# Performance work log

Hardware: AMD Instinct MI355X
Metric: run time of the kernel (lower is better)

Reference implementation:

```python
import math
import jax, jax.numpy as jnp
import numpy as np

B, S, HID, H, NREL = 4, 512, 1024, 16, 64
D = HID // H  # per-head size = 64, must equal relation embedding dim


def setup_inputs() -> dict:
    key = jax.random.key(0)
    ks = jax.random.split(key, 12)
    w = lambda k, shape: jax.random.normal(k, shape, jnp.float32) * 0.02
    return {
        "q_in": jax.random.normal(ks[0], (B, S, HID), jnp.float32),
        "k_in": jax.random.normal(ks[1], (B, S, HID), jnp.float32),
        "v_in": jax.random.normal(ks[2], (B, S, HID), jnp.float32),
        "mask": jax.random.randint(ks[3], (B, 1, S, S), 0, NREL),
        "Wq": w(ks[4], (HID, HID)), "bq": jnp.zeros((HID,), jnp.float32),
        "Wk": w(ks[5], (HID, HID)), "bk": jnp.zeros((HID,), jnp.float32),
        "Wv": w(ks[6], (HID, HID)), "bv": jnp.zeros((HID,), jnp.float32),
        "Wo": w(ks[7], (HID, HID)), "bo": jnp.zeros((HID,), jnp.float32),
        "rel_k_table": w(ks[8], (NREL, D)),
        "rel_v_table": w(ks[9], (NREL, D)),
    }


def reference(q_in, k_in, v_in, mask, Wq, bq, Wk, bk, Wv, bv, Wo, bo,
              rel_k_table, rel_v_table):
    def proj(x, W, b):  # [B,S,HID] -> [B,H,S,D]
        return (x @ W.T + b).reshape(B, S, H, D).transpose(0, 2, 1, 3)

    q = proj(q_in, Wq, bq)
    k = proj(k_in, Wk, bk)
    v = proj(v_in, Wv, bv)

    ids = mask[:, 0]                      # [B,S,S] relation ids
    rel_k = rel_k_table[ids]              # [B,S,S,D]
    rel_v = rel_v_table[ids]              # [B,S,S,D]

    scores = jnp.einsum('bhqd,bhkd->bhqk', q, k)
    scores = scores + jnp.einsum('bhqd,bqkd->bhqk', q, rel_k) / 4.0
    scores = scores / math.sqrt(float(D))

    bias = (1.0 - (mask > 0).astype(scores.dtype)) * -10000.0  # [B,1,S,S]
    probs = jax.nn.softmax(scores + bias, axis=-1)             # [B,H,S,S]

    out = jnp.einsum('bhqk,bhkd->bhqd', probs, v)
    out = out + 0.25 * jnp.einsum('bhqk,bqkd->bhqd', probs, rel_v)
    out = out.transpose(0, 2, 1, 3).reshape(B, S, HID)
    return out @ Wo.T + bo
```

## Files before the change

kernel.cpp:

```cpp
#include <hip/hip_runtime.h>


typedef __attribute__((ext_vector_type(8))) short bf16x8 __attribute__((may_alias));
typedef __attribute__((ext_vector_type(4))) float f32x4;

__device__ __forceinline__ short f2bf(float x) {
    unsigned u = __float_as_uint(x);
    u += 0x7fff + ((u >> 16) & 1);
    return (short)(u >> 16);
}

__device__ __forceinline__ void async16(void* lds, const void* g) {
    __builtin_amdgcn_global_load_lds(
        (const __attribute__((address_space(1))) void*)g,
        (__attribute__((address_space(3))) void*)lds, 16, 0, 0);
}

__global__ __launch_bounds__(256)
void cast_all(const float* __restrict__ x0, const float* __restrict__ x1, const float* __restrict__ x2,
              const float* __restrict__ w0, const float* __restrict__ w1,
              const float* __restrict__ w2, const float* __restrict__ w3,
              short* __restrict__ y0, short* __restrict__ y1, short* __restrict__ y2,
              short* __restrict__ u0, short* __restrict__ u1,
              short* __restrict__ u2, short* __restrict__ u3)
{
    size_t i = (size_t)blockIdx.x * 256 + threadIdx.x;
    const float* src; short* dst; size_t off;
    if (i < 3u*524288u) {
        int s = (int)(i / 524288u); off = i % 524288u;
        src = s == 0 ? x0 : (s == 1 ? x1 : x2);
        dst = s == 0 ? y0 : (s == 1 ? y1 : y2);
    } else {
        size_t j = i - 3u*524288u;
        int s = (int)(j / 262144u); off = j % 262144u;
        src = s == 0 ? w0 : (s == 1 ? w1 : (s == 2 ? w2 : w3));
        dst = s == 0 ? u0 : (s == 1 ? u1 : (s == 2 ? u2 : u3));
    }
    float4 f = ((const float4*)src)[off];
    short4 o; o.x = f2bf(f.x); o.y = f2bf(f.y); o.z = f2bf(f.z); o.w = f2bf(f.w);
    ((short4*)dst)[off] = o;
}

__global__ __launch_bounds__(256)
void gemm12864(const short* __restrict__ A0, const short* __restrict__ A1, const short* __restrict__ A2,
               const short* __restrict__ B0, const short* __restrict__ B1, const short* __restrict__ B2,
               const float* __restrict__ c0, const float* __restrict__ c1, const float* __restrict__ c2,
               void* __restrict__ O0, void* __restrict__ O1, void* __restrict__ O2,
               int mode)
{
    __shared__ short ldsw[2 * 12288];

    const int z = blockIdx.z;
    const short* A    = z == 0 ? A0 : (z == 1 ? A1 : A2);
    const short* Bm   = z == 0 ? B0 : (z == 1 ? B1 : B2);
    const float* bias = z == 0 ? c0 : (z == 1 ? c1 : c2);
    void*        O    = z == 0 ? O0 : (z == 1 ? O1 : O2);

    const int t = threadIdx.x;
    const int lane = t & 63, w = t >> 6;
    const int wr = w >> 1, wc = w & 1;
    const int quad = lane >> 4, cl = lane & 15;
    const int rowBase = blockIdx.y * 128;
    const int colBase = blockIdx.x * 64;
    const int gl = ((lane & 7) - (lane >> 3)) & 7;

    f32x4 acc[4][2];
#pragma unroll
    for (int i = 0; i < 4; ++i)
#pragma unroll
        for (int j = 0; j < 2; ++j) acc[i][j] = (f32x4){0.f, 0.f, 0.f, 0.f};

    const int rstage = w * 8 + (lane >> 3);
    const short* Ag = A  + (size_t)(rowBase + rstage) * 1024 + gl * 8;
    const short* Bg = Bm + (size_t)(colBase + rstage) * 1024 + gl * 8;

    {
        short* Als = ldsw;
        short* Bls = ldsw + 8192;
#pragma unroll
        for (int i = 0; i < 4; ++i)
            async16(&Als[(i * 32 + w * 8) * 64], Ag + (size_t)i * 32 * 1024);
#pragma unroll
        for (int i = 0; i < 2; ++i)
            async16(&Bls[(i * 32 + w * 8) * 64], Bg + (size_t)i * 32 * 1024);
    }

    for (int it = 0; it < 16; ++it) {
        const int cur = it & 1;
        __syncthreads();
        if (it < 15) {
            short* Als = ldsw + (cur ^ 1) * 12288;
            short* Bls = Als + 8192;
            const int k0 = (it + 1) * 64;
#pragma unroll
            for (int i = 0; i < 4; ++i)
                async16(&Als[(i * 32 + w * 8) * 64], Ag + (size_t)i * 32 * 1024 + k0);
#pragma unroll
            for (int i = 0; i < 2; ++i)
                async16(&Bls[(i * 32 + w * 8) * 64], Bg + (size_t)i * 32 * 1024 + k0);
        }
        const short* Als = ldsw + cur * 12288;
        const short* Bls = Als + 8192;
#pragma unroll
        for (int kk = 0; kk < 2; ++kk) {
            bf16x8 a[4], b[2];
#pragma unroll
            for (int mi = 0; mi < 4; ++mi) {
                int r = wr * 64 + mi * 16 + cl;
                int s = (kk * 4 + quad + r) & 7;
                a[mi] = *(const bf16x8*)&Als[r * 64 + s * 8];
            }
#pragma unroll
            for (int ni = 0; ni < 2; ++ni) {
                int r = wc * 32 + ni * 16 + cl;
                int s = (kk * 4 + quad + r) & 7;
                b[ni] = *(const bf16x8*)&Bls[r * 64 + s * 8];
            }
#pragma unroll
            for (int mi = 0; mi < 4; ++mi)
#pragma unroll
                for (int ni = 0; ni < 2; ++ni)
                    acc[mi][ni] = __builtin_amdgcn_mfma_f32_16x16x32_bf16(
                        a[mi], b[ni], acc[mi][ni], 0, 0, 0);
        }
    }

    if (mode == 0) {
#pragma unroll
        for (int mi = 0; mi < 4; ++mi)
#pragma unroll
            for (int ni = 0; ni < 2; ++ni) {
                int col = colBase + wc * 32 + ni * 16 + cl;
                float bv = bias[col];
#pragma unroll
                for (int reg = 0; reg < 4; ++reg) {
                    int row = rowBase + wr * 64 + mi * 16 + quad * 4 + reg;
                    ((float*)O)[(size_t)row * 1024 + col] = acc[mi][ni][reg] + bv;
                }
            }
        return;
    }

    __syncthreads();
    short* Tls = ldsw;
    if (z == 2) {
#pragma unroll
        for (int mi = 0; mi < 4; ++mi)
#pragma unroll
            for (int ni = 0; ni < 2; ++ni) {
                int d = wc * 32 + ni * 16 + cl;
                float bv = bias[colBase + d];
                short4 pk;
                pk.x = f2bf(acc[mi][ni][0] + bv);
                pk.y = f2bf(acc[mi][ni][1] + bv);
                pk.z = f2bf(acc[mi][ni][2] + bv);
                pk.w = f2bf(acc[mi][ni][3] + bv);
                int sl = wr * 64 + mi * 16 + quad * 4;
                *(short4*)&Tls[d * 136 + sl] = pk;
            }
        __syncthreads();
        int d = t >> 2, s0 = (t & 3) * 32;
        int bb = rowBase >> 9, sBase = rowBase & 511, hh = colBase >> 6;
        short* dst = (short*)O + (((size_t)(bb * 16 + hh) * 64 + d) << 9) + sBase + s0;
#pragma unroll
        for (int j = 0; j < 4; ++j)
            *(bf16x8*)(dst + j * 8) = *(const bf16x8*)&Tls[d * 136 + s0 + j * 8];
    } else {
#pragma unroll
        for (int mi = 0; mi < 4; ++mi)
#pragma unroll
            for (int ni = 0; ni < 2; ++ni) {
                int d = wc * 32 + ni * 16 + cl;
                float bv = bias[colBase + d];
#pragma unroll
                for (int reg = 0; reg < 4; ++reg) {
                    int sl = wr * 64 + mi * 16 + quad * 4 + reg;
                    Tls[sl * 72 + d] = f2bf(acc[mi][ni][reg] + bv);
                }
            }
        __syncthreads();
        int sl = t >> 1, half = t & 1;
        int bb = rowBase >> 9, sBase = rowBase & 511, hh = colBase >> 6;
        short* dst = (short*)O + (((size_t)(bb * 16 + hh) * 512 + sBase + sl) << 6) + half * 32;
#pragma unroll
        for (int j = 0; j < 4; ++j)
            *(bf16x8*)(dst + j * 8) = *(const bf16x8*)&Tls[sl * 72 + half * 32 + j * 8];
    }
}

#define AT_BINS 4352
#define AT_PST  8704
#define AT_TOT  11264

__global__ __launch_bounds__(64)
void attn_kernel(const short* __restrict__ qg, const short* __restrict__ kg,
                 const short* __restrict__ vtg, const int* __restrict__ mask,
                 const float* __restrict__ relk, const float* __restrict__ relv,
                 short* __restrict__ attn_b)
{
    __shared__ __align__(16) char pool[AT_TOT];
    float* qwr    = (float*)pool;
    float* bins   = (float*)(pool + AT_BINS);
    short* Pst    = (short*)(pool + AT_PST);
    short* binsBf = Pst;

    const int lane = threadIdx.x;
    const int quad = lane >> 4, cl = lane & 15;
    const int bid = blockIdx.x;
    const int bh = bid & 63, qbk = bid >> 6;
    const int b = bh >> 4, h = bh & 15, q0 = qbk * 16;

    const short* qbase = qg  + ((size_t)bh * 512 + q0) * 64;
    const short* kbase = kg  + (size_t)bh * 512 * 64;
    const short* vbase = vtg + (size_t)bh * 64 * 512;
    const int*   mb    = mask + (size_t)b * 512 * 512 + (size_t)q0 * 512;

    for (int i = lane; i < 16 * 68; i += 64) bins[i] = 0.f;

    bf16x8 qa0 = *(const bf16x8*)(qbase + cl * 64 + quad * 8);
    bf16x8 qa1 = *(const bf16x8*)(qbase + cl * 64 + 32 + quad * 8);

#pragma unroll
    for (int rt = 0; rt < 4; ++rt) {
        const float* kp = relk + (size_t)(rt * 16 + cl) * 64 + quad * 8;
        bf16x8 rb0, rb1;
#pragma unroll
        for (int j = 0; j < 8; ++j) rb0[j] = f2bf(kp[j]);
#pragma unroll
        for (int j = 0; j < 8; ++j) rb1[j] = f2bf(kp[32 + j]);
        f32x4 qr = (f32x4){0.f, 0.f, 0.f, 0.f};
        qr = __builtin_amdgcn_mfma_f32_16x16x32_bf16(qa0, rb0, qr, 0, 0, 0);
        qr = __builtin_amdgcn_mfma_f32_16x16x32_bf16(qa1, rb1, qr, 0, 0, 0);
#pragma unroll
        for (int reg = 0; reg < 4; ++reg)
            qwr[(quad * 4 + reg) * 68 + rt * 16 + cl] = qr[reg];
    }

    f32x4 oacc[4];
#pragma unroll
    for (int dt = 0; dt < 4; ++dt) oacc[dt] = (f32x4){0.f, 0.f, 0.f, 0.f};
    float lpart[4] = {0.f, 0.f, 0.f, 0.f};

    for (int c = 0; c < 8; ++c) {
        const int k0 = c * 64;
#pragma unroll
        for (int nt = 0; nt < 4; ++nt) {
            const int kidx = k0 + nt * 16 + cl;
            const short* kp = kbase + (size_t)kidx * 64 + quad * 8;
            bf16x8 kb0 = *(const bf16x8*)kp;
            bf16x8 kb1 = *(const bf16x8*)(kp + 32);
            f32x4 s = (f32x4){0.f, 0.f, 0.f, 0.f};
            s = __builtin_amdgcn_mfma_f32_16x16x32_bf16(qa0, kb0, s, 0, 0, 0);
            s = __builtin_amdgcn_mfma_f32_16x16x32_bf16(qa1, kb1, s, 0, 0, 0);
#pragma unroll
            for (int reg = 0; reg < 4; ++reg) {
                int q = quad * 4 + reg;
                int id = mb[q * 512 + kidx];
                float sc = (s[reg] + 0.25f * qwr[q * 68 + id]) * 0.125f;
                float p = (id == 0) ? 0.f : __expf(sc);
                lpart[reg] += p;
                atomicAdd(&bins[q * 68 + id], p);
                Pst[q * 72 + nt * 16 + cl] = f2bf(p);
            }
        }
        bf16x8 pa0 = *(const bf16x8*)&Pst[cl * 72 + quad * 8];
        bf16x8 pa1 = *(const bf16x8*)&Pst[cl * 72 + 32 + quad * 8];
#pragma unroll
        for (int dt = 0; dt < 4; ++dt) {
            const short* vp = vbase + (size_t)(dt * 16 + cl) * 512 + k0 + quad * 8;
            bf16x8 vb0 = *(const bf16x8*)vp;
            bf16x8 vb1 = *(const bf16x8*)(vp + 32);
            oacc[dt] = __builtin_amdgcn_mfma_f32_16x16x32_bf16(pa0, vb0, oacc[dt], 0, 0, 0);
            oacc[dt] = __builtin_amdgcn_mfma_f32_16x16x32_bf16(pa1, vb1, oacc[dt], 0, 0, 0);
        }
    }

    float invq[4];
#pragma unroll
    for (int reg = 0; reg < 4; ++reg) {
        float l = lpart[reg];
#pragma unroll
        for (int m = 8; m >= 1; m >>= 1) l += __shfl_xor(l, m);
        invq[reg] = 1.0f / l;
    }

    {
        int q = lane >> 2, r0 = (lane & 3) * 16;
#pragma unroll
        for (int j = 0; j < 4; ++j) {
            float4 f = *(const float4*)&bins[q * 68 + r0 + j * 4];
            short4 o;
            o.x = f2bf(f.x); o.y = f2bf(f.y); o.z = f2bf(f.z); o.w = f2bf(f.w);
            *(short4*)&binsBf[q * 72 + r0 + j * 4] = o;
        }
    }

    bf16x8 ba0 = *(const bf16x8*)&binsBf[cl * 72 + quad * 8];
    bf16x8 ba1 = *(const bf16x8*)&binsBf[cl * 72 + 32 + quad * 8];
#pragma unroll
    for (int dt = 0; dt < 4; ++dt) {
        const float* rp = relv + (size_t)(quad * 8) * 64 + dt * 16 + cl;
        bf16x8 rv0, rv1;
#pragma unroll
        for (int j = 0; j < 8; ++j) rv0[j] = f2bf(rp[j * 64]);
#pragma unroll
        for (int j = 0; j < 8; ++j) rv1[j] = f2bf(rp[2048 + j * 64]);
        f32x4 racc = (f32x4){0.f, 0.f, 0.f, 0.f};
        racc = __builtin_amdgcn_mfma_f32_16x16x32_bf16(ba0, rv0, racc, 0, 0, 0);
        racc = __builtin_amdgcn_mfma_f32_16x16x32_bf16(ba1, rv1, racc, 0, 0, 0);
#pragma unroll
        for (int reg = 0; reg < 4; ++reg) {
            int q = quad * 4 + reg;
            float val = (oacc[dt][reg] + 0.25f * racc[reg]) * invq[reg];
            attn_b[(size_t)(b * 512 + q0 + q) * 1024 + h * 64 + dt * 16 + cl] = f2bf(val);
        }
    }
}

extern "C" void kernel_launch(void* const* d_in, const int* in_sizes, int n_in,
                              void* d_out, int out_size, void* d_ws, size_t ws_size,
                              hipStream_t stream)
{
    const float* q_in = (const float*)d_in[0];
    const float* k_in = (const float*)d_in[1];
    const float* v_in = (const float*)d_in[2];
    const int*   mask = (const int*)d_in[3];
    const float* Wq   = (const float*)d_in[4];
    const float* bq   = (const float*)d_in[5];
    const float* Wk   = (const float*)d_in[6];
    const float* bk   = (const float*)d_in[7];
    const float* Wv   = (const float*)d_in[8];
    const float* bv   = (const float*)d_in[9];
    const float* Wo   = (const float*)d_in[10];
    const float* bo   = (const float*)d_in[11];
    const float* relk = (const float*)d_in[12];
    const float* relv = (const float*)d_in[13];

    char* ws = (char*)d_ws;
    short* qb     = (short*)(ws);
    short* kb     = (short*)(ws + (4u  << 20));
    short* vt     = (short*)(ws + (8u  << 20));
    short* attn_b = (short*)(ws + (12u << 20));
    short* Xq     = (short*)(ws + (16u << 20));
    short* Xk     = (short*)(ws + (20u << 20));
    short* Xv     = (short*)(ws + (24u << 20));
    short* Wqb    = (short*)(ws + (28u << 20));
    short* Wkb    = (short*)(ws + (30u << 20));
    short* Wvb    = (short*)(ws + (32u << 20));
    short* Wob    = (short*)(ws + (34u << 20));

    cast_all<<<10240, 256, 0, stream>>>(q_in, k_in, v_in, Wq, Wk, Wv, Wo,
                                        Xq, Xk, Xv, Wqb, Wkb, Wvb, Wob);

    gemm12864<<<dim3(16, 16, 3), 256, 0, stream>>>(
        Xq, Xk, Xv, Wqb, Wkb, Wvb, bq, bk, bv, qb, kb, vt, 1);

    attn_kernel<<<dim3(2048), 64, 0, stream>>>(qb, kb, vt, mask, relk, relv, attn_b);

    gemm12864<<<dim3(16, 16, 1), 256, 0, stream>>>(
        attn_b, attn_b, attn_b, Wob, Wob, Wob, bo, bo, bo,
        (void*)d_out, (void*)d_out, (void*)d_out, 0);
}
```

Baseline: 239.7 us.

## Split attention key range across four waves and precast relation tables

The attention kernel now runs four 64-lane waves per block instead of one. Each wave handles a quarter of the 512 keys and gets its own P staging buffer, and the partial outputs and row sums are combined through LDS atomics and block barriers. The relation-key and relation-value tables are converted to bf16 (the value table also transposed) once inside the cast kernel, so each attention block no longer does strided fp32 loads and conversions. Mask ids for a chunk are prefetched into registers before the score MFMAs. The aim is more parallelism per query tile and less serial latency, at the cost of extra syncs and LDS atomic reductions.

```diff
diff --git a/kernel.cpp b/kernel.cpp
--- a/kernel.cpp
+++ b/kernel.cpp
@@ -20,25 +20,43 @@
 void cast_all(const float* __restrict__ x0, const float* __restrict__ x1, const float* __restrict__ x2,
               const float* __restrict__ w0, const float* __restrict__ w1,
               const float* __restrict__ w2, const float* __restrict__ w3,
+              const float* __restrict__ rk, const float* __restrict__ rv,
               short* __restrict__ y0, short* __restrict__ y1, short* __restrict__ y2,
               short* __restrict__ u0, short* __restrict__ u1,
-              short* __restrict__ u2, short* __restrict__ u3)
+              short* __restrict__ u2, short* __restrict__ u3,
+              short* __restrict__ rkb, short* __restrict__ rvT)
 {
     size_t i = (size_t)blockIdx.x * 256 + threadIdx.x;
-    const float* src; short* dst; size_t off;
-    if (i < 3u*524288u) {
-        int s = (int)(i / 524288u); off = i % 524288u;
-        src = s == 0 ? x0 : (s == 1 ? x1 : x2);
-        dst = s == 0 ? y0 : (s == 1 ? y1 : y2);
+    if (i < 2621440u) {
+        const float* src; short* dst; size_t off;
+        if (i < 3u*524288u) {
+            int s = (int)(i / 524288u); off = i % 524288u;
+            src = s == 0 ? x0 : (s == 1 ? x1 : x2);
+            dst = s == 0 ? y0 : (s == 1 ? y1 : y2);
+        } else {
+            size_t j = i - 3u*524288u;
+            int s = (int)(j / 262144u); off = j % 262144u;
+            src = s == 0 ? w0 : (s == 1 ? w1 : (s == 2 ? w2 : w3));
+            dst = s == 0 ? u0 : (s == 1 ? u1 : (s == 2 ? u2 : u3));
+        }
+        float4 f = ((const float4*)src)[off];
+        short4 o; o.x = f2bf(f.x); o.y = f2bf(f.y); o.z = f2bf(f.z); o.w = f2bf(f.w);
+        ((short4*)dst)[off] = o;
+    } else if (i < 2621440u + 1024u) {
+        size_t off = i - 2621440u;
+        float4 f = ((const float4*)rk)[off];
+        short4 o; o.x = f2bf(f.x); o.y = f2bf(f.y); o.z = f2bf(f.z); o.w = f2bf(f.w);
+        ((short4*)rkb)[off] = o;
     } else {
-        size_t j = i - 3u*524288u;
-        int s = (int)(j / 262144u); off = j % 262144u;
-        src = s == 0 ? w0 : (s == 1 ? w1 : (s == 2 ? w2 : w3));
-        dst = s == 0 ? u0 : (s == 1 ? u1 : (s == 2 ? u2 : u3));
-    }
-    float4 f = ((const float4*)src)[off];
-    short4 o; o.x = f2bf(f.x); o.y = f2bf(f.y); o.z = f2bf(f.z); o.w = f2bf(f.w);
-    ((short4*)dst)[off] = o;
+        int m = (int)(i - 2622464u);
+        int d = m >> 4, r0 = (m & 15) * 4;
+        short4 o;
+        o.x = f2bf(rv[(size_t)(r0 + 0) * 64 + d]);
+        o.y = f2bf(rv[(size_t)(r0 + 1) * 64 + d]);
+        o.z = f2bf(rv[(size_t)(r0 + 2) * 64 + d]);
+        o.w = f2bf(rv[(size_t)(r0 + 3) * 64 + d]);
+        *(short4*)&rvT[d * 64 + r0] = o;
+    }
 }
 
 __global__ __launch_bounds__(256)
@@ -188,23 +206,26 @@
     }
 }
 
+#define AT_QWR  0
 #define AT_BINS 4352
-#define AT_PST  8704
-#define AT_TOT  11264
-
-__global__ __launch_bounds__(64)
+#define AT_LSUM 8704
+#define AT_PST  8768
+#define AT_TOT  (8768 + 4 * 2304)
+
+__global__ __launch_bounds__(256, 4)
 void attn_kernel(const short* __restrict__ qg, const short* __restrict__ kg,
                  const short* __restrict__ vtg, const int* __restrict__ mask,
-                 const float* __restrict__ relk, const float* __restrict__ relv,
+                 const short* __restrict__ relkb, const short* __restrict__ relvT,
                  short* __restrict__ attn_b)
 {
     __shared__ __align__(16) char pool[AT_TOT];
-    float* qwr    = (float*)pool;
-    float* bins   = (float*)(pool + AT_BINS);
-    short* Pst    = (short*)(pool + AT_PST);
-    short* binsBf = Pst;
-
-    const int lane = threadIdx.x;
+    float* qwr  = (float*)(pool + AT_QWR);
+    float* bins = (float*)(pool + AT_BINS);
+    float* lsum = (float*)(pool + AT_LSUM);
+    short* Pst  = (short*)(pool + AT_PST);
+
+    const int t = threadIdx.x;
+    const int lane = t & 63, w = t >> 6;
     const int quad = lane >> 4, cl = lane & 15;
     const int bid = blockIdx.x;
     const int bh = bid & 63, qbk = bid >> 6;
@@ -215,34 +236,41 @@
     const short* vbase = vtg + (size_t)bh * 64 * 512;
     const int*   mb    = mask + (size_t)b * 512 * 512 + (size_t)q0 * 512;
 
-    for (int i = lane; i < 16 * 68; i += 64) bins[i] = 0.f;
+    for (int i = t; i < 16 * 68; i += 256) bins[i] = 0.f;
+    if (t < 16) lsum[t] = 0.f;
 
     bf16x8 qa0 = *(const bf16x8*)(qbase + cl * 64 + quad * 8);
     bf16x8 qa1 = *(const bf16x8*)(qbase + cl * 64 + 32 + quad * 8);
 
-#pragma unroll
-    for (int rt = 0; rt < 4; ++rt) {
-        const float* kp = relk + (size_t)(rt * 16 + cl) * 64 + quad * 8;
-        bf16x8 rb0, rb1;
-#pragma unroll
-        for (int j = 0; j < 8; ++j) rb0[j] = f2bf(kp[j]);
-#pragma unroll
-        for (int j = 0; j < 8; ++j) rb1[j] = f2bf(kp[32 + j]);
+    {
+        const short* kp = relkb + (size_t)(w * 16 + cl) * 64 + quad * 8;
+        bf16x8 rb0 = *(const bf16x8*)kp;
+        bf16x8 rb1 = *(const bf16x8*)(kp + 32);
         f32x4 qr = (f32x4){0.f, 0.f, 0.f, 0.f};
         qr = __builtin_amdgcn_mfma_f32_16x16x32_bf16(qa0, rb0, qr, 0, 0, 0);
         qr = __builtin_amdgcn_mfma_f32_16x16x32_bf16(qa1, rb1, qr, 0, 0, 0);
 #pragma unroll
         for (int reg = 0; reg < 4; ++reg)
-            qwr[(quad * 4 + reg) * 68 + rt * 16 + cl] = qr[reg];
-    }
+            qwr[(quad * 4 + reg) * 68 + w * 16 + cl] = qr[reg];
+    }
+    __syncthreads();
 
     f32x4 oacc[4];
 #pragma unroll
     for (int dt = 0; dt < 4; ++dt) oacc[dt] = (f32x4){0.f, 0.f, 0.f, 0.f};
     float lpart[4] = {0.f, 0.f, 0.f, 0.f};
-
-    for (int c = 0; c < 8; ++c) {
-        const int k0 = c * 64;
+    short* myPst = Pst + w * 1152;
+
+#pragma unroll
+    for (int cc = 0; cc < 2; ++cc) {
+        const int k0 = (w * 2 + cc) * 64;
+        int ids[4][4];
+#pragma unroll
+        for (int nt = 0; nt < 4; ++nt)
+#pragma unroll
+            for (int reg = 0; reg < 4; ++reg)
+                ids[nt][reg] = mb[(size_t)(quad * 4 + reg) * 512 + k0 + nt * 16 + cl];
+
 #pragma unroll
         for (int nt = 0; nt < 4; ++nt) {
             const int kidx = k0 + nt * 16 + cl;
@@ -255,16 +283,16 @@
 #pragma unroll
             for (int reg = 0; reg < 4; ++reg) {
                 int q = quad * 4 + reg;
-                int id = mb[q * 512 + kidx];
+                int id = ids[nt][reg];
                 float sc = (s[reg] + 0.25f * qwr[q * 68 + id]) * 0.125f;
                 float p = (id == 0) ? 0.f : __expf(sc);
                 lpart[reg] += p;
                 atomicAdd(&bins[q * 68 + id], p);
-                Pst[q * 72 + nt * 16 + cl] = f2bf(p);
+                myPst[q * 72 + nt * 16 + cl] = f2bf(p);
             }
         }
-        bf16x8 pa0 = *(const bf16x8*)&Pst[cl * 72 + quad * 8];
-        bf16x8 pa1 = *(const bf16x8*)&Pst[cl * 72 + 32 + quad * 8];
+        bf16x8 pa0 = *(const bf16x8*)&myPst[cl * 72 + quad * 8];
+        bf16x8 pa1 = *(const bf16x8*)&myPst[cl * 72 + 32 + quad * 8];
 #pragma unroll
         for (int dt = 0; dt < 4; ++dt) {
             const short* vp = vbase + (size_t)(dt * 16 + cl) * 512 + k0 + quad * 8;
@@ -275,45 +303,53 @@
         }
     }
 
-    float invq[4];
 #pragma unroll
     for (int reg = 0; reg < 4; ++reg) {
         float l = lpart[reg];
 #pragma unroll
         for (int m = 8; m >= 1; m >>= 1) l += __shfl_xor(l, m);
-        invq[reg] = 1.0f / l;
-    }
+        lpart[reg] = l;
+    }
+    if ((lane & 15) == 0) {
+#pragma unroll
+        for (int reg = 0; reg < 4; ++reg)
+            atomicAdd(&lsum[quad * 4 + reg], lpart[reg]);
+    }
+    __syncthreads();
+
+    float* obuf   = (float*)(pool + AT_PST);
+    short* binsBf = (short*)(pool + AT_PST + 4352);
+    for (int i = t; i < 16 * 68; i += 256) obuf[i] = 0.f;
+    __syncthreads();
+#pragma unroll
+    for (int dt = 0; dt < 4; ++dt)
+#pragma unroll
+        for (int reg = 0; reg < 4; ++reg)
+            atomicAdd(&obuf[(quad * 4 + reg) * 68 + dt * 16 + cl], oacc[dt][reg]);
+    __syncthreads();
 
     {
-        int q = lane >> 2, r0 = (lane & 3) * 16;
-#pragma unroll
-        for (int j = 0; j < 4; ++j) {
-            float4 f = *(const float4*)&bins[q * 68 + r0 + j * 4];
-            short4 o;
-            o.x = f2bf(f.x); o.y = f2bf(f.y); o.z = f2bf(f.z); o.w = f2bf(f.w);
-            *(short4*)&binsBf[q * 72 + r0 + j * 4] = o;
-        }
-    }
+        int row = t >> 4, c0 = (t & 15) * 4;
+        float4 f = *(const float4*)&bins[row * 68 + c0];
+        short4 o;
+        o.x = f2bf(f.x); o.y = f2bf(f.y); o.z = f2bf(f.z); o.w = f2bf(f.w);
+        *(short4*)&binsBf[row * 72 + c0] = o;
+    }
+    __syncthreads();
 
     bf16x8 ba0 = *(const bf16x8*)&binsBf[cl * 72 + quad * 8];
     bf16x8 ba1 = *(const bf16x8*)&binsBf[cl * 72 + 32 + quad * 8];
-#pragma unroll
-    for (int dt = 0; dt < 4; ++dt) {
-        const float* rp = relv + (size_t)(quad * 8) * 64 + dt * 16 + cl;
-        bf16x8 rv0, rv1;
-#pragma unroll
-        for (int j = 0; j < 8; ++j) rv0[j] = f2bf(rp[j * 64]);
-#pragma unroll
-        for (int j = 0; j < 8; ++j) rv1[j] = f2bf(rp[2048 + j * 64]);
-        f32x4 racc = (f32x4){0.f, 0.f, 0.f, 0.f};
-        racc = __builtin_amdgcn_mfma_f32_16x16x32_bf16(ba0, rv0, racc, 0, 0, 0);
-        racc = __builtin_amdgcn_mfma_f32_16x16x32_bf16(ba1, rv1, racc, 0, 0, 0);
-#pragma unroll
-        for (int reg = 0; reg < 4; ++reg) {
-            int q = quad * 4 + reg;
-            float val = (oacc[dt][reg] + 0.25f * racc[reg]) * invq[reg];
-            attn_b[(size_t)(b * 512 + q0 + q) * 1024 + h * 64 + dt * 16 + cl] = f2bf(val);
-        }
+    const short* rp = relvT + (size_t)(w * 16 + cl) * 64 + quad * 8;
+    bf16x8 rv0 = *(const bf16x8*)rp;
+    bf16x8 rv1 = *(const bf16x8*)(rp + 32);
+    f32x4 racc = (f32x4){0.f, 0.f, 0.f, 0.f};
+    racc = __builtin_amdgcn_mfma_f32_16x16x32_bf16(ba0, rv0, racc, 0, 0, 0);
+    racc = __builtin_amdgcn_mfma_f32_16x16x32_bf16(ba1, rv1, racc, 0, 0, 0);
+#pragma unroll
+    for (int reg = 0; reg < 4; ++reg) {
+        int q = quad * 4 + reg;
+        float val = (obuf[q * 68 + w * 16 + cl] + 0.25f * racc[reg]) / lsum[q];
+        attn_b[(size_t)(b * 512 + q0 + q) * 1024 + h * 64 + w * 16 + cl] = f2bf(val);
     }
 }
 
@@ -348,14 +384,16 @@
     short* Wkb    = (short*)(ws + (30u << 20));
     short* Wvb    = (short*)(ws + (32u << 20));
     short* Wob    = (short*)(ws + (34u << 20));
-
-    cast_all<<<10240, 256, 0, stream>>>(q_in, k_in, v_in, Wq, Wk, Wv, Wo,
-                                        Xq, Xk, Xv, Wqb, Wkb, Wvb, Wob);
+    short* relkb  = (short*)(ws + (36u << 20));
+    short* relvT  = (short*)(ws + (36u << 20) + 8192);
+
+    cast_all<<<10248, 256, 0, stream>>>(q_in, k_in, v_in, Wq, Wk, Wv, Wo, relk, relv,
+                                        Xq, Xk, Xv, Wqb, Wkb, Wvb, Wob, relkb, relvT);
 
     gemm12864<<<dim3(16, 16, 3), 256, 0, stream>>>(
         Xq, Xk, Xv, Wqb, Wkb, Wvb, bq, bk, bv, qb, kb, vt, 1);
 
-    attn_kernel<<<dim3(2048), 64, 0, stream>>>(qb, kb, vt, mask, relk, relv, attn_b);
+    attn_kernel<<<dim3(2048), 256, 0, stream>>>(qb, kb, vt, mask, relkb, relvT, attn_b);
 
     gemm12864<<<dim3(16, 16, 1), 256, 0, stream>>>(
         attn_b, attn_b, attn_b, Wob, Wob, Wob, bo, bo, bo,
```

New measurement: 276.2 us. 1.15x slower.

## Prefetch K and mask tiles in attention, pre-cast relation tables to bf16

Applied to the files above, without the earlier changes.

The attention loop now double-buffers K fragments and mask ids in registers, issuing the loads for the next 64-key chunk while the current chunk is computed. V fragments and the relation-key gathers are also issued early in each iteration. The relation tables are converted to bf16 (rel_v also transposed) once inside the cast kernel, so each attention block no longer does scalar fp32 loads and conversions. A launch-bounds hint is added. This raises register pressure, which could reduce occupancy or cause spills.

```diff
diff --git a/kernel.cpp b/kernel.cpp
--- a/kernel.cpp
+++ b/kernel.cpp
@@ -20,25 +20,43 @@
 void cast_all(const float* __restrict__ x0, const float* __restrict__ x1, const float* __restrict__ x2,
               const float* __restrict__ w0, const float* __restrict__ w1,
               const float* __restrict__ w2, const float* __restrict__ w3,
+              const float* __restrict__ rk, const float* __restrict__ rv,
               short* __restrict__ y0, short* __restrict__ y1, short* __restrict__ y2,
               short* __restrict__ u0, short* __restrict__ u1,
-              short* __restrict__ u2, short* __restrict__ u3)
+              short* __restrict__ u2, short* __restrict__ u3,
+              short* __restrict__ rkb, short* __restrict__ rvT)
 {
     size_t i = (size_t)blockIdx.x * 256 + threadIdx.x;
-    const float* src; short* dst; size_t off;
-    if (i < 3u*524288u) {
-        int s = (int)(i / 524288u); off = i % 524288u;
-        src = s == 0 ? x0 : (s == 1 ? x1 : x2);
-        dst = s == 0 ? y0 : (s == 1 ? y1 : y2);
+    if (i < 2621440u) {
+        const float* src; short* dst; size_t off;
+        if (i < 3u*524288u) {
+            int s = (int)(i / 524288u); off = i % 524288u;
+            src = s == 0 ? x0 : (s == 1 ? x1 : x2);
+            dst = s == 0 ? y0 : (s == 1 ? y1 : y2);
+        } else {
+            size_t j = i - 3u*524288u;
+            int s = (int)(j / 262144u); off = j % 262144u;
+            src = s == 0 ? w0 : (s == 1 ? w1 : (s == 2 ? w2 : w3));
+            dst = s == 0 ? u0 : (s == 1 ? u1 : (s == 2 ? u2 : u3));
+        }
+        float4 f = ((const float4*)src)[off];
+        short4 o; o.x = f2bf(f.x); o.y = f2bf(f.y); o.z = f2bf(f.z); o.w = f2bf(f.w);
+        ((short4*)dst)[off] = o;
+    } else if (i < 2621440u + 1024u) {
+        size_t off = i - 2621440u;
+        float4 f = ((const float4*)rk)[off];
+        short4 o; o.x = f2bf(f.x); o.y = f2bf(f.y); o.z = f2bf(f.z); o.w = f2bf(f.w);
+        ((short4*)rkb)[off] = o;
     } else {
-        size_t j = i - 3u*524288u;
-        int s = (int)(j / 262144u); off = j % 262144u;
-        src = s == 0 ? w0 : (s == 1 ? w1 : (s == 2 ? w2 : w3));
-        dst = s == 0 ? u0 : (s == 1 ? u1 : (s == 2 ? u2 : u3));
-    }
-    float4 f = ((const float4*)src)[off];
-    short4 o; o.x = f2bf(f.x); o.y = f2bf(f.y); o.z = f2bf(f.z); o.w = f2bf(f.w);
-    ((short4*)dst)[off] = o;
+        int m = (int)(i - 2622464u);
+        int d = m >> 4, r0 = (m & 15) * 4;
+        short4 o;
+        o.x = f2bf(rv[(size_t)(r0 + 0) * 64 + d]);
+        o.y = f2bf(rv[(size_t)(r0 + 1) * 64 + d]);
+        o.z = f2bf(rv[(size_t)(r0 + 2) * 64 + d]);
+        o.w = f2bf(rv[(size_t)(r0 + 3) * 64 + d]);
+        *(short4*)&rvT[d * 64 + r0] = o;
+    }
 }
 
 __global__ __launch_bounds__(256)
@@ -192,10 +210,10 @@
 #define AT_PST  8704
 #define AT_TOT  11264
 
-__global__ __launch_bounds__(64)
+__global__ __launch_bounds__(64, 2)
 void attn_kernel(const short* __restrict__ qg, const short* __restrict__ kg,
                  const short* __restrict__ vtg, const int* __restrict__ mask,
-                 const float* __restrict__ relk, const float* __restrict__ relv,
+                 const short* __restrict__ relkb, const short* __restrict__ relvT,
                  short* __restrict__ attn_b)
 {
     __shared__ __align__(16) char pool[AT_TOT];
@@ -220,14 +238,25 @@
     bf16x8 qa0 = *(const bf16x8*)(qbase + cl * 64 + quad * 8);
     bf16x8 qa1 = *(const bf16x8*)(qbase + cl * 64 + 32 + quad * 8);
 
+    bf16x8 kbuf[2][8];
+    int    idb[2][16];
+#pragma unroll
+    for (int nt = 0; nt < 4; ++nt) {
+        const short* kp = kbase + (size_t)(nt * 16 + cl) * 64 + quad * 8;
+        kbuf[0][nt * 2]     = *(const bf16x8*)kp;
+        kbuf[0][nt * 2 + 1] = *(const bf16x8*)(kp + 32);
+    }
+#pragma unroll
+    for (int nt = 0; nt < 4; ++nt)
+#pragma unroll
+        for (int reg = 0; reg < 4; ++reg)
+            idb[0][nt * 4 + reg] = mb[(size_t)(quad * 4 + reg) * 512 + nt * 16 + cl];
+
 #pragma unroll
     for (int rt = 0; rt < 4; ++rt) {
-        const float* kp = relk + (size_t)(rt * 16 + cl) * 64 + quad * 8;
-        bf16x8 rb0, rb1;
-#pragma unroll
-        for (int j = 0; j < 8; ++j) rb0[j] = f2bf(kp[j]);
-#pragma unroll
-        for (int j = 0; j < 8; ++j) rb1[j] = f2bf(kp[32 + j]);
+        const short* kp = relkb + (size_t)(rt * 16 + cl) * 64 + quad * 8;
+        bf16x8 rb0 = *(const bf16x8*)kp;
+        bf16x8 rb1 = *(const bf16x8*)(kp + 32);
         f32x4 qr = (f32x4){0.f, 0.f, 0.f, 0.f};
         qr = __builtin_amdgcn_mfma_f32_16x16x32_bf16(qa0, rb0, qr, 0, 0, 0);
         qr = __builtin_amdgcn_mfma_f32_16x16x32_bf16(qa1, rb1, qr, 0, 0, 0);
@@ -241,22 +270,49 @@
     for (int dt = 0; dt < 4; ++dt) oacc[dt] = (f32x4){0.f, 0.f, 0.f, 0.f};
     float lpart[4] = {0.f, 0.f, 0.f, 0.f};
 
+#pragma unroll
     for (int c = 0; c < 8; ++c) {
+        const int cur = c & 1, nxt = cur ^ 1;
         const int k0 = c * 64;
+
+        float qv[16];
+#pragma unroll
+        for (int e = 0; e < 16; ++e)
+            qv[e] = qwr[(quad * 4 + (e & 3)) * 68 + idb[cur][e]];
+
+        bf16x8 vb[8];
+#pragma unroll
+        for (int dt = 0; dt < 4; ++dt) {
+            const short* vp = vbase + (size_t)(dt * 16 + cl) * 512 + k0 + quad * 8;
+            vb[dt * 2]     = *(const bf16x8*)vp;
+            vb[dt * 2 + 1] = *(const bf16x8*)(vp + 32);
+        }
+
+        if (c < 7) {
+            const int k1 = k0 + 64;
+#pragma unroll
+            for (int nt = 0; nt < 4; ++nt) {
+                const short* kp = kbase + (size_t)(k1 + nt * 16 + cl) * 64 + quad * 8;
+                kbuf[nxt][nt * 2]     = *(const bf16x8*)kp;
+                kbuf[nxt][nt * 2 + 1] = *(const bf16x8*)(kp + 32);
+            }
+#pragma unroll
+            for (int nt = 0; nt < 4; ++nt)
+#pragma unroll
+                for (int reg = 0; reg < 4; ++reg)
+                    idb[nxt][nt * 4 + reg] = mb[(size_t)(quad * 4 + reg) * 512 + k1 + nt * 16 + cl];
+        }
+
 #pragma unroll
         for (int nt = 0; nt < 4; ++nt) {
-            const int kidx = k0 + nt * 16 + cl;
-            const short* kp = kbase + (size_t)kidx * 64 + quad * 8;
-            bf16x8 kb0 = *(const bf16x8*)kp;
-            bf16x8 kb1 = *(const bf16x8*)(kp + 32);
             f32x4 s = (f32x4){0.f, 0.f, 0.f, 0.f};
-            s = __builtin_amdgcn_mfma_f32_16x16x32_bf16(qa0, kb0, s, 0, 0, 0);
-            s = __builtin_amdgcn_mfma_f32_16x16x32_bf16(qa1, kb1, s, 0, 0, 0);
+            s = __builtin_amdgcn_mfma_f32_16x16x32_bf16(qa0, kbuf[cur][nt * 2],     s, 0, 0, 0);
+            s = __builtin_amdgcn_mfma_f32_16x16x32_bf16(qa1, kbuf[cur][nt * 2 + 1], s, 0, 0, 0);
 #pragma unroll
             for (int reg = 0; reg < 4; ++reg) {
                 int q = quad * 4 + reg;
-                int id = mb[q * 512 + kidx];
-                float sc = (s[reg] + 0.25f * qwr[q * 68 + id]) * 0.125f;
+                int id = idb[cur][nt * 4 + reg];
+                float sc = fmaf(qv[nt * 4 + reg], 0.03125f, s[reg] * 0.125f);
                 float p = (id == 0) ? 0.f : __expf(sc);
                 lpart[reg] += p;
                 atomicAdd(&bins[q * 68 + id], p);
@@ -267,11 +323,8 @@
         bf16x8 pa1 = *(const bf16x8*)&Pst[cl * 72 + 32 + quad * 8];
 #pragma unroll
         for (int dt = 0; dt < 4; ++dt) {
-            const short* vp = vbase + (size_t)(dt * 16 + cl) * 512 + k0 + quad * 8;
-            bf16x8 vb0 = *(const bf16x8*)vp;
-            bf16x8 vb1 = *(const bf16x8*)(vp + 32);
-            oacc[dt] = __builtin_amdgcn_mfma_f32_16x16x32_bf16(pa0, vb0, oacc[dt], 0, 0, 0);
-            oacc[dt] = __builtin_amdgcn_mfma_f32_16x16x32_bf16(pa1, vb1, oacc[dt], 0, 0, 0);
+            oacc[dt] = __builtin_amdgcn_mfma_f32_16x16x32_bf16(pa0, vb[dt * 2],     oacc[dt], 0, 0, 0);
+            oacc[dt] = __builtin_amdgcn_mfma_f32_16x16x32_bf16(pa1, vb[dt * 2 + 1], oacc[dt], 0, 0, 0);
         }
     }
 
@@ -299,12 +352,9 @@
     bf16x8 ba1 = *(const bf16x8*)&binsBf[cl * 72 + 32 + quad * 8];
 #pragma unroll
     for (int dt = 0; dt < 4; ++dt) {
-        const float* rp = relv + (size_t)(quad * 8) * 64 + dt * 16 + cl;
-        bf16x8 rv0, rv1;
-#pragma unroll
-        for (int j = 0; j < 8; ++j) rv0[j] = f2bf(rp[j * 64]);
-#pragma unroll
-        for (int j = 0; j < 8; ++j) rv1[j] = f2bf(rp[2048 + j * 64]);
+        const short* rp = relvT + (size_t)(dt * 16 + cl) * 64 + quad * 8;
+        bf16x8 rv0 = *(const bf16x8*)rp;
+        bf16x8 rv1 = *(const bf16x8*)(rp + 32);
         f32x4 racc = (f32x4){0.f, 0.f, 0.f, 0.f};
         racc = __builtin_amdgcn_mfma_f32_16x16x32_bf16(ba0, rv0, racc, 0, 0, 0);
         racc = __builtin_amdgcn_mfma_f32_16x16x32_bf16(ba1, rv1, racc, 0, 0, 0);
@@ -348,14 +398,16 @@
     short* Wkb    = (short*)(ws + (30u << 20));
     short* Wvb    = (short*)(ws + (32u << 20));
     short* Wob    = (short*)(ws + (34u << 20));
-
-    cast_all<<<10240, 256, 0, stream>>>(q_in, k_in, v_in, Wq, Wk, Wv, Wo,
-                                        Xq, Xk, Xv, Wqb, Wkb, Wvb, Wob);
+    short* relkb  = (short*)(ws + (36u << 20));
+    short* relvT  = (short*)(ws + (36u << 20) + 8192);
+
+    cast_all<<<10248, 256, 0, stream>>>(q_in, k_in, v_in, Wq, Wk, Wv, Wo, relk, relv,
+                                        Xq, Xk, Xv, Wqb, Wkb, Wvb, Wob, relkb, relvT);
 
     gemm12864<<<dim3(16, 16, 3), 256, 0, stream>>>(
         Xq, Xk, Xv, Wqb, Wkb, Wvb, bq, bk, bv, qb, kb, vt, 1);
 
-    attn_kernel<<<dim3(2048), 64, 0, stream>>>(qb, kb, vt, mask, relk, relv, attn_b);
+    attn_kernel<<<dim3(2048), 64, 0, stream>>>(qb, kb, vt, mask, relkb, relvT, attn_b);
 
     gemm12864<<<dim3(16, 16, 1), 256, 0, stream>>>(
         attn_b, attn_b, attn_b, Wob, Wob, Wob, bo, bo, bo,
```

Measured after the change: 245.9 us. 1.03x slower.
